# Optimization experiments

Measured on AMD Instinct MI355X. Metric: run time of the kernel, lower is better.

## Reference

```python
import jax, jax.numpy as jnp
import numpy as np

D_MODEL = 1024
NUM_HEADS = 16
DEPTH = D_MODEL // NUM_HEADS


def setup_inputs() -> dict:
    key = jax.random.key(0)
    ks = jax.random.split(key, 11)
    B, S = 4, 2048
    scale = 1.0 / np.sqrt(D_MODEL)
    inp = {
        "q": jax.random.normal(ks[0], (B, S, D_MODEL), jnp.float32),
        "k": jax.random.normal(ks[1], (B, S, D_MODEL), jnp.float32),
        "v": jax.random.normal(ks[2], (B, S, D_MODEL), jnp.float32),
        # Linear params (weight stored [out, in] like torch; applied as x @ W.T + b)
        "wq_w": jax.random.normal(ks[3], (D_MODEL, D_MODEL), jnp.float32) * scale,
        "wq_b": jnp.zeros((D_MODEL,), jnp.float32),
        "wk_w": jax.random.normal(ks[4], (D_MODEL, D_MODEL), jnp.float32) * scale,
        "wk_b": jnp.zeros((D_MODEL,), jnp.float32),
        "wv_w": jax.random.normal(ks[5], (D_MODEL, D_MODEL), jnp.float32) * scale,
        "wv_b": jnp.zeros((D_MODEL,), jnp.float32),
        "wo_w": jax.random.normal(ks[6], (D_MODEL, D_MODEL), jnp.float32) * scale,
        "wo_b": jnp.zeros((D_MODEL,), jnp.float32),
    }
    return inp


def _split_heads(x, B, S):
    # [B, S, D] -> [B, H, S, depth]
    return x.reshape(B, S, NUM_HEADS, DEPTH).transpose(0, 2, 1, 3)


def reference(q, k, v, wq_w, wq_b, wk_w, wk_b, wv_w, wv_b, wo_w, wo_b):
    B, S, _ = q.shape
    qh = _split_heads(q @ wq_w.T + wq_b, B, S)
    kh = _split_heads(k @ wk_w.T + wk_b, B, S)
    vh = _split_heads(v @ wv_w.T + wv_b, B, S)
    # scaled dot-product attention: [B, H, Sq, Sk]
    scores = jnp.einsum("bhqd,bhkd->bhqk", qh, kh) / jnp.sqrt(
        jnp.asarray(DEPTH, qh.dtype))
    attn = jax.nn.softmax(scores, axis=-1)
    ctx = jnp.einsum("bhqk,bhkd->bhqd", attn, vh)
    # [B, H, S, depth] -> [B, S, D]
    ctx = ctx.transpose(0, 2, 1, 3).reshape(B, S, D_MODEL)
    return ctx @ wo_w.T + wo_b
```

## Files before the change

kernel.cpp:

```cpp
#include <hip/hip_runtime.h>
#include <hip/hip_bf16.h>

typedef __attribute__((ext_vector_type(8))) short bf16x8;
typedef __attribute__((ext_vector_type(4))) short bf16x4;
typedef __attribute__((ext_vector_type(4))) float f32x4;
typedef __attribute__((address_space(3))) ushort lds_ushort;

#define MFMA32(a, b, c) __builtin_amdgcn_mfma_f32_16x16x32_bf16(a, b, c, 0, 0, 0)
#if __has_builtin(__builtin_amdgcn_mfma_f32_16x16x16bf16_1k)
#define HAVE_MFMA16K 1
#define MFMA16K(a, b, c) __builtin_amdgcn_mfma_f32_16x16x16bf16_1k(a, b, c, 0, 0, 0)
#else
#define HAVE_MFMA16K 0
#endif

#define ASYNC16(g, l)                                                          \
    __builtin_amdgcn_global_load_lds(                                          \
        (const __attribute__((address_space(1))) unsigned int*)(g),            \
        (__attribute__((address_space(3))) unsigned int*)(l), 16, 0, 0)

#define TR16(dst, addr, OFF)                                                   \
    asm volatile("ds_read_b64_tr_b16 %0, %1 offset:%2"                         \
                 : "=v"(dst) : "v"(addr), "i"(OFF))

__device__ __forceinline__ ushort f2bf(float f) {
    __hip_bfloat16 h = __float2bfloat16(f);
    return *reinterpret_cast<ushort*>(&h);
}
__device__ __forceinline__ uint cvtpk(float a, float b) {
    uint r;
    asm("v_cvt_pk_bf16_f32 %0, %1, %2" : "=v"(r) : "v"(a), "v"(b));
    return r;
}

#define QSCALE 0.18033688011112042f

struct CvtArgs { const float* s[7]; ushort* d[7]; int nb[7]; };

__global__ __launch_bounds__(256) void cvtk(CvtArgs a) {
    const int z = blockIdx.y;
    if ((int)blockIdx.x >= a.nb[z]) return;
    const float* s = a.s[z];
    ushort* d = a.d[z];
    const size_t i = (size_t)blockIdx.x * 2048 + threadIdx.x * 8;
    float4 f0 = *(const float4*)&s[i];
    float4 f1 = *(const float4*)&s[i + 4];
    *(ushort4*)&d[i]     = make_ushort4(f2bf(f0.x), f2bf(f0.y), f2bf(f0.z), f2bf(f0.w));
    *(ushort4*)&d[i + 4] = make_ushort4(f2bf(f1.x), f2bf(f1.y), f2bf(f1.z), f2bf(f1.w));
}

struct GemmArgs {
    const ushort* X[3]; const ushort* W[3]; const float* B[3];
    void* O[3]; int mode[3]; float scale[3];
};

__global__ __launch_bounds__(256) void gemm3(GemmArgs g) {
    __shared__ __attribute__((aligned(16))) ushort As[2][128][32];
    __shared__ __attribute__((aligned(16))) ushort Bs[2][128][32];

    const int z = blockIdx.z;
    const ushort* __restrict__ X = g.X[z];
    const ushort* __restrict__ W = g.W[z];
    const float*  __restrict__ bias = g.B[z];
    const int mode = g.mode[z];
    const float scale = g.scale[z];

    const int tid  = threadIdx.x;
    const int lane = tid & 63;
    const int wave = tid >> 6;
    const int quad = lane >> 4;
    const int l16  = lane & 15;
    const int wm   = (wave >> 1) * 64;
    const int wn   = (wave & 1) * 64;

    const int flat = blockIdx.x + 8 * blockIdx.y;
    const int t    = (flat & 7) * 64 + (flat >> 3);
    const int m0   = (t >> 3) * 128;
    const int n0   = (t & 7) * 128;

    f32x4 acc[4][4];
#pragma unroll
    for (int i = 0; i < 4; i++)
#pragma unroll
        for (int j = 0; j < 4; j++) acc[i][j] = (f32x4)0.0f;

    auto stage = [&](int buf, int k0) {
#pragma unroll
        for (int j = 0; j < 2; j++) {
            const int c   = j * 256 + tid;
            const int r   = c >> 2;
            const int col = (c & 3) * 8;
            ASYNC16(&X[(size_t)(m0 + r) * 1024 + k0 + col],
                    &As[buf][0][0] + (size_t)(j * 256 + wave * 64) * 8);
            ASYNC16(&W[(size_t)(n0 + r) * 1024 + k0 + col],
                    &Bs[buf][0][0] + (size_t)(j * 256 + wave * 64) * 8);
        }
    };

    stage(0, 0);
    stage(1, 32);
    int cur = 0;

    for (int k0 = 0; k0 < 1024; k0 += 32) {
        if (k0 < 1024 - 32) {
            asm volatile("s_waitcnt vmcnt(4)" ::: "memory");
        } else {
            asm volatile("s_waitcnt vmcnt(0)" ::: "memory");
        }
        __builtin_amdgcn_s_barrier();
        __builtin_amdgcn_sched_barrier(0);

        bf16x8 af[4], bfr[4];
#pragma unroll
        for (int i = 0; i < 4; i++)
            af[i] = *(const bf16x8*)&As[cur][wm + i * 16 + l16][quad * 8];
#pragma unroll
        for (int j = 0; j < 4; j++)
            bfr[j] = *(const bf16x8*)&Bs[cur][wn + j * 16 + l16][quad * 8];
        asm volatile("s_waitcnt lgkmcnt(0)" ::: "memory");
        __builtin_amdgcn_sched_barrier(0);
        __builtin_amdgcn_s_barrier();
        __builtin_amdgcn_sched_barrier(0);
        if (k0 + 64 < 1024) stage(cur, k0 + 64);

#pragma unroll
        for (int i = 0; i < 4; i++)
#pragma unroll
            for (int j = 0; j < 4; j++)
                acc[i][j] = MFMA32(af[i], bfr[j], acc[i][j]);
        cur ^= 1;
    }

#pragma unroll
    for (int i = 0; i < 4; i++) {
#pragma unroll
        for (int j = 0; j < 4; j++) {
            const int n  = n0 + wn + j * 16 + l16;
            const float bb = bias[n];
#pragma unroll
            for (int r = 0; r < 4; r++) {
                const int m = m0 + wm + i * 16 + quad * 4 + r;
                const float val = (acc[i][j][r] + bb) * scale;
                if (mode == 2) {
                    ((float*)g.O[z])[(size_t)m * 1024 + n] = val;
                } else {
                    const int bat = m >> 11, s = m & 2047, h = n >> 6, d = n & 63;
                    ((ushort*)g.O[z])[((size_t)((bat * 16 + h) * 2048 + s)) * 64 + d]
                        = f2bf(val);
                }
            }
        }
    }
}

__global__ __launch_bounds__(256, 4) void attn(
    const ushort* __restrict__ Qp, const ushort* __restrict__ Kp,
    const ushort* __restrict__ Vp, ushort* __restrict__ ctx)
{
    __shared__ __attribute__((aligned(16))) ushort Ks[2][2 * 64 * 32];
    __shared__ __attribute__((aligned(16))) ushort Vs[2][64 * 64];

    const int tid  = threadIdx.x;
    const int lane = tid & 63;
    const int wave = tid >> 6;
    const int quad = lane >> 4;
    const int l16  = lane & 15;

    const int id = blockIdx.x;
    const int bh = (id & 7) * 8 + ((id >> 3) & 7);
    const int q0 = (id >> 6) * 128;
    const int b  = bh >> 4, h = bh & 15;

    const ushort* Qg = Qp + ((size_t)bh * 2048 + q0) * 64;
    const ushort* Kg = Kp + (size_t)bh * 2048 * 64;
    const ushort* Vg = Vp + (size_t)bh * 2048 * 64;

    bf16x8 aq[2][2];
#pragma unroll
    for (int st = 0; st < 2; st++)
#pragma unroll
        for (int kk = 0; kk < 2; kk++)
            aq[st][kk] = *(const bf16x8*)&Qg[(size_t)(wave * 32 + st * 16 + l16) * 64
                                            + kk * 32 + quad * 8];

    f32x4 o[2][4];
#pragma unroll
    for (int st = 0; st < 2; st++)
#pragma unroll
        for (int jd = 0; jd < 4; jd++) o[st][jd] = (f32x4)0.0f;
#if HAVE_MFMA16K
    f32x4 ls[2] = {(f32x4)0.0f, (f32x4)0.0f};
    union { uint u[2]; bf16x4 v; } ones;
    ones.u[0] = 0x3F803F80u; ones.u[1] = 0x3F803F80u;
#else
    float lsum[2] = {0.f, 0.f};
#endif

    auto stage = [&](int buf, int n0) {
#pragma unroll
        for (int j = 0; j < 2; j++) {
            const int c    = j * 256 + tid;
            const int colq = c & 3;
            const int row  = (c >> 2) & 63;
            const int half = c >> 8;
            ASYNC16(&Kg[(size_t)(n0 + row) * 64 + half * 32 + colq * 8],
                    &Ks[buf][0] + (size_t)(j * 256 + wave * 64) * 8);
        }
#pragma unroll
        for (int j = 0; j < 2; j++) {
            const int c   = j * 256 + tid;
            const int key = ((c >> 5) << 2) | ((c >> 1) & 3);
            const int d   = (((c >> 3) & 3) << 4) | ((c & 1) << 3);
            ASYNC16(&Vg[(size_t)(n0 + key) * 64 + d],
                    &Vs[buf][0] + (size_t)(j * 256 + wave * 64) * 8);
        }
    };

    stage(0, 0);
    int cur = 0;

    for (int n0 = 0; n0 < 2048; n0 += 64) {
        __syncthreads();
        if (n0 + 64 < 2048) stage(cur ^ 1, n0 + 64);

        uint pk[4][2][2];
#pragma unroll
        for (int kb = 0; kb < 4; kb++) {
            bf16x8 kf0 = *(const bf16x8*)&Ks[cur][(size_t)(kb * 16 + l16) * 32 + quad * 8];
            bf16x8 kf1 = *(const bf16x8*)&Ks[cur][(size_t)(64 + kb * 16 + l16) * 32 + quad * 8];
#pragma unroll
            for (int st = 0; st < 2; st++) {
                f32x4 s = (f32x4)0.0f;
                s = MFMA32(kf0, aq[st][0], s);
                s = MFMA32(kf1, aq[st][1], s);
                float e0 = __builtin_amdgcn_exp2f(s[0]);
                float e1 = __builtin_amdgcn_exp2f(s[1]);
                float e2 = __builtin_amdgcn_exp2f(s[2]);
                float e3 = __builtin_amdgcn_exp2f(s[3]);
                pk[kb][st][0] = cvtpk(e0, e1);
                pk[kb][st][1] = cvtpk(e2, e3);
#if !HAVE_MFMA16K
                lsum[st] += (e0 + e1) + (e2 + e3);
#endif
            }
        }

#if HAVE_MFMA16K
        const lds_ushort* vp = (const lds_ushort*)&Vs[cur][0] + quad * 256 + l16 * 4;
        bf16x4 vf[4][4];
#define TRISSUE(JD)                                                            \
        TR16(vf[JD][0], vp, (JD) * 128 + 0);                                   \
        TR16(vf[JD][1], vp, (JD) * 128 + 2048);                                \
        TR16(vf[JD][2], vp, (JD) * 128 + 4096);                                \
        TR16(vf[JD][3], vp, (JD) * 128 + 6144);
        TRISSUE(0) TRISSUE(1) TRISSUE(2) TRISSUE(3)

#pragma unroll
        for (int kb = 0; kb < 4; kb++) {
#pragma unroll
            for (int st = 0; st < 2; st++) {
                union { uint u[2]; bf16x4 v; } pf;
                pf.u[0] = pk[kb][st][0];
                pf.u[1] = pk[kb][st][1];
                ls[st] = MFMA16K(pf.v, ones.v, ls[st]);
            }
        }

#define PVWAIT(N)                                                              \
        asm volatile("s_waitcnt lgkmcnt(" #N ")" ::: "memory");                \
        __builtin_amdgcn_sched_barrier(0);
#define PVJD(JD)                                                               \
        _Pragma("unroll")                                                      \
        for (int kb = 0; kb < 4; kb++) {                                       \
            _Pragma("unroll")                                                  \
            for (int st = 0; st < 2; st++) {                                   \
                union { uint u[2]; bf16x4 v; } pf;                             \
                pf.u[0] = pk[kb][st][0];                                       \
                pf.u[1] = pk[kb][st][1];                                       \
                o[st][JD] = MFMA16K(pf.v, vf[JD][kb], o[st][JD]);              \
            }                                                                  \
        }
        __builtin_amdgcn_s_setprio(1);
        PVWAIT(12) PVJD(0)
        PVWAIT(8)  PVJD(1)
        PVWAIT(4)  PVJD(2)
        PVWAIT(0)  PVJD(3)
        __builtin_amdgcn_s_setprio(0);
#else
        const int addr0 = 4 * ((2 * (quad & 1)) * 16 + l16);
        const int addr1 = addr0 + 64;
#pragma unroll
        for (int kt = 0; kt < 2; kt++) {
            bf16x8 apf[2];
#pragma unroll
            for (int st = 0; st < 2; st++) {
                union { uint u[4]; bf16x8 v; } t;
#pragma unroll
                for (int j = 0; j < 4; j++) {
                    uint src = (quad & 2) ? pk[kt * 2 + 1][st][j & 1]
                                          : pk[kt * 2][st][j & 1];
                    t.u[j] = (uint)__builtin_amdgcn_ds_bpermute(
                        (j >> 1) ? addr1 : addr0, (int)src);
                }
                apf[st] = t.v;
            }
#pragma unroll
            for (int jd = 0; jd < 4; jd++) {
                union { ushort s[8]; bf16x8 v; } vv;
#pragma unroll
                for (int e = 0; e < 8; e++) {
                    const int key = kt * 32 + quad * 8 + e;
                    const int d   = jd * 16 + l16;
                    vv.s[e] = Vs[cur][(key >> 2) * 256 + (d >> 4) * 64
                                      + (key & 3) * 16 + (d & 15)];
                }
#pragma unroll
                for (int st = 0; st < 2; st++)
                    o[st][jd] = MFMA32(apf[st], vv.v, o[st][jd]);
            }
        }
#endif
        cur ^= 1;
    }

#if HAVE_MFMA16K
#pragma unroll
    for (int st = 0; st < 2; st++) {
        float inv[4];
#pragma unroll
        for (int r = 0; r < 4; r++) inv[r] = 1.0f / ls[st][r];
#pragma unroll
        for (int jd = 0; jd < 4; jd++) {
#pragma unroll
            for (int r = 0; r < 4; r++) {
                const int s = q0 + wave * 32 + st * 16 + quad * 4 + r;
                ctx[((size_t)(b * 2048 + s)) * 1024 + h * 64 + jd * 16 + l16] =
                    f2bf(o[st][jd][r] * inv[r]);
            }
        }
    }
#else
#pragma unroll
    for (int st = 0; st < 2; st++) {
        float lsv = lsum[st];
        lsv += __shfl_xor(lsv, 16, 64);
        lsv += __shfl_xor(lsv, 32, 64);
        float inv[4];
#pragma unroll
        for (int r = 0; r < 4; r++)
            inv[r] = 1.0f / __shfl(lsv, quad * 4 + r, 64);
#pragma unroll
        for (int jd = 0; jd < 4; jd++) {
#pragma unroll
            for (int r = 0; r < 4; r++) {
                const int s = q0 + wave * 32 + st * 16 + quad * 4 + r;
                ctx[((size_t)(b * 2048 + s)) * 1024 + h * 64 + jd * 16 + l16] =
                    f2bf(o[st][jd][r] * inv[r]);
            }
        }
    }
#endif
}

extern "C" void kernel_launch(void* const* d_in, const int* in_sizes, int n_in,
                              void* d_out, int out_size, void* d_ws, size_t ws_size,
                              hipStream_t stream) {
    const float* q    = (const float*)d_in[0];
    const float* k    = (const float*)d_in[1];
    const float* v    = (const float*)d_in[2];
    const float* wq_w = (const float*)d_in[3];
    const float* wq_b = (const float*)d_in[4];
    const float* wk_w = (const float*)d_in[5];
    const float* wk_b = (const float*)d_in[6];
    const float* wv_w = (const float*)d_in[7];
    const float* wv_b = (const float*)d_in[8];
    const float* wo_w = (const float*)d_in[9];
    const float* wo_b = (const float*)d_in[10];
    float* out = (float*)d_out;

    const size_t NE = (size_t)4 * 2048 * 1024;
    const size_t NW = (size_t)1024 * 1024;
    const size_t need_fused = (6 * NE + 4 * NW) * 2;

    dim3 blk(256);

    if (ws_size >= need_fused) {
        ushort* Xq = (ushort*)d_ws;
        ushort* Xk = Xq + NE;
        ushort* Xv = Xk + NE;
        ushort* Wq = Xv + NE;
        ushort* Wk = Wq + NW;
        ushort* Wv = Wk + NW;
        ushort* Wo = Wv + NW;
        ushort* Qp = Wo + NW;
        ushort* Kp = Qp + NE;
        ushort* Vp = Kp + NE;
        ushort* ctx = Xq;

        CvtArgs ca;
        ca.s[0]=q;    ca.d[0]=Xq; ca.nb[0]=4096;
        ca.s[1]=k;    ca.d[1]=Xk; ca.nb[1]=4096;
        ca.s[2]=v;    ca.d[2]=Xv; ca.nb[2]=4096;
        ca.s[3]=wq_w; ca.d[3]=Wq; ca.nb[3]=512;
        ca.s[4]=wk_w; ca.d[4]=Wk; ca.nb[4]=512;
        ca.s[5]=wv_w; ca.d[5]=Wv; ca.nb[5]=512;
        ca.s[6]=wo_w; ca.d[6]=Wo; ca.nb[6]=512;
        cvtk<<<dim3(4096, 7), blk, 0, stream>>>(ca);

        GemmArgs ga;
        ga.X[0]=Xq; ga.W[0]=Wq; ga.B[0]=wq_b; ga.O[0]=Qp; ga.mode[0]=0; ga.scale[0]=QSCALE;
        ga.X[1]=Xk; ga.W[1]=Wk; ga.B[1]=wk_b; ga.O[1]=Kp; ga.mode[1]=0; ga.scale[1]=1.0f;
        ga.X[2]=Xv; ga.W[2]=Wv; ga.B[2]=wv_b; ga.O[2]=Vp; ga.mode[2]=0; ga.scale[2]=1.0f;
        gemm3<<<dim3(8, 64, 3), blk, 0, stream>>>(ga);

        attn<<<dim3(1024), blk, 0, stream>>>(Qp, Kp, Vp, ctx);

        GemmArgs go;
        go.X[0]=ctx; go.W[0]=Wo; go.B[0]=wo_b; go.O[0]=out; go.mode[0]=2; go.scale[0]=1.0f;
        go.X[1]=go.X[0]; go.W[1]=go.W[0]; go.B[1]=go.B[0]; go.O[1]=go.O[0]; go.mode[1]=2; go.scale[1]=1.0f;
        go.X[2]=go.X[0]; go.W[2]=go.W[0]; go.B[2]=go.B[0]; go.O[2]=go.O[0]; go.mode[2]=2; go.scale[2]=1.0f;
        gemm3<<<dim3(8, 64, 1), blk, 0, stream>>>(go);
    } else {
        ushort* Xb  = (ushort*)d_ws;
        ushort* Wb  = Xb + NE;
        ushort* Wob = Wb + NW;
        ushort* Qp  = Wob + NW;
        ushort* Kp  = Qp + NE;
        ushort* Vp  = Kp + NE;
        ushort* ctx = Xb;

        CvtArgs c0;
        c0.s[0]=q;    c0.d[0]=Xb;  c0.nb[0]=4096;
        c0.s[1]=wq_w; c0.d[1]=Wb;  c0.nb[1]=512;
        c0.s[2]=wo_w; c0.d[2]=Wob; c0.nb[2]=512;
        for (int i = 3; i < 7; i++) { c0.s[i]=q; c0.d[i]=Xb; c0.nb[i]=0; }
        cvtk<<<dim3(4096, 3), blk, 0, stream>>>(c0);
        GemmArgs ga;
        for (int i = 0; i < 3; i++) { ga.X[i]=Xb; ga.W[i]=Wb; ga.B[i]=wq_b; ga.O[i]=Qp; ga.mode[i]=0; ga.scale[i]=QSCALE; }
        gemm3<<<dim3(8, 64, 1), blk, 0, stream>>>(ga);

        CvtArgs c1;
        c1.s[0]=k;    c1.d[0]=Xb; c1.nb[0]=4096;
        c1.s[1]=wk_w; c1.d[1]=Wb; c1.nb[1]=512;
        for (int i = 2; i < 7; i++) { c1.s[i]=k; c1.d[i]=Xb; c1.nb[i]=0; }
        cvtk<<<dim3(4096, 2), blk, 0, stream>>>(c1);
        GemmArgs gb;
        for (int i = 0; i < 3; i++) { gb.X[i]=Xb; gb.W[i]=Wb; gb.B[i]=wk_b; gb.O[i]=Kp; gb.mode[i]=0; gb.scale[i]=1.0f; }
        gemm3<<<dim3(8, 64, 1), blk, 0, stream>>>(gb);

        CvtArgs c2;
        c2.s[0]=v;    c2.d[0]=Xb; c2.nb[0]=4096;
        c2.s[1]=wv_w; c2.d[1]=Wb; c2.nb[1]=512;
        for (int i = 2; i < 7; i++) { c2.s[i]=v; c2.d[i]=Xb; c2.nb[i]=0; }
        cvtk<<<dim3(4096, 2), blk, 0, stream>>>(c2);
        GemmArgs gc;
        for (int i = 0; i < 3; i++) { gc.X[i]=Xb; gc.W[i]=Wb; gc.B[i]=wv_b; gc.O[i]=Vp; gc.mode[i]=0; gc.scale[i]=1.0f; }
        gemm3<<<dim3(8, 64, 1), blk, 0, stream>>>(gc);

        attn<<<dim3(1024), blk, 0, stream>>>(Qp, Kp, Vp, ctx);

        GemmArgs go;
        for (int i = 0; i < 3; i++) { go.X[i]=ctx; go.W[i]=Wob; go.B[i]=wo_b; go.O[i]=out; go.mode[i]=2; go.scale[i]=1.0f; }
        gemm3<<<dim3(8, 64, 1), blk, 0, stream>>>(go);
    }
}
```

Baseline: 338.4 us.

## Fuse fp32-to-bf16 activation conversion into QKV projection GEMM loads

The separate conversion pass over the q/k/v activations is removed. The QKV GEMM now loads fp32 rows directly, converts them to bf16 in registers with packed cvt, and writes them into LDS, prefetching one tile ahead. Only the weights are still pre-converted. This removes a full write and reread of three activation tensors, but the A operand now goes through registers instead of async global-to-LDS loads. The bf16 GEMM path also drops its hand-tuned vmcnt waits in favour of a simpler __syncthreads double buffer, which may add stalls.

```diff
diff --git a/kernel.cpp b/kernel.cpp
--- a/kernel.cpp
+++ b/kernel.cpp
@@ -35,7 +35,7 @@
 
 #define QSCALE 0.18033688011112042f
 
-struct CvtArgs { const float* s[7]; ushort* d[7]; int nb[7]; };
+struct CvtArgs { const float* s[4]; ushort* d[4]; int nb[4]; };
 
 __global__ __launch_bounds__(256) void cvtk(CvtArgs a) {
     const int z = blockIdx.y;
@@ -50,8 +50,8 @@
 }
 
 struct GemmArgs {
-    const ushort* X[3]; const ushort* W[3]; const float* B[3];
-    void* O[3]; int mode[3]; float scale[3];
+    const ushort* X[3]; const float* Xf[3]; const ushort* W[3];
+    const float* B[3]; void* O[3]; int mode[3]; int xf32[3]; float scale[3];
 };
 
 __global__ __launch_bounds__(256) void gemm3(GemmArgs g) {
@@ -59,7 +59,6 @@
     __shared__ __attribute__((aligned(16))) ushort Bs[2][128][32];
 
     const int z = blockIdx.z;
-    const ushort* __restrict__ X = g.X[z];
     const ushort* __restrict__ W = g.W[z];
     const float*  __restrict__ bias = g.B[z];
     const int mode = g.mode[z];
@@ -84,51 +83,100 @@
 #pragma unroll
         for (int j = 0; j < 4; j++) acc[i][j] = (f32x4)0.0f;
 
-    auto stage = [&](int buf, int k0) {
+    auto stageB = [&](int buf, int k0) {
 #pragma unroll
         for (int j = 0; j < 2; j++) {
             const int c   = j * 256 + tid;
             const int r   = c >> 2;
             const int col = (c & 3) * 8;
-            ASYNC16(&X[(size_t)(m0 + r) * 1024 + k0 + col],
-                    &As[buf][0][0] + (size_t)(j * 256 + wave * 64) * 8);
             ASYNC16(&W[(size_t)(n0 + r) * 1024 + k0 + col],
                     &Bs[buf][0][0] + (size_t)(j * 256 + wave * 64) * 8);
         }
     };
 
-    stage(0, 0);
-    stage(1, 32);
-    int cur = 0;
-
-    for (int k0 = 0; k0 < 1024; k0 += 32) {
-        if (k0 < 1024 - 32) {
-            asm volatile("s_waitcnt vmcnt(4)" ::: "memory");
-        } else {
-            asm volatile("s_waitcnt vmcnt(0)" ::: "memory");
-        }
-        __builtin_amdgcn_s_barrier();
-        __builtin_amdgcn_sched_barrier(0);
-
-        bf16x8 af[4], bfr[4];
-#pragma unroll
-        for (int i = 0; i < 4; i++)
-            af[i] = *(const bf16x8*)&As[cur][wm + i * 16 + l16][quad * 8];
-#pragma unroll
-        for (int j = 0; j < 4; j++)
-            bfr[j] = *(const bf16x8*)&Bs[cur][wn + j * 16 + l16][quad * 8];
-        asm volatile("s_waitcnt lgkmcnt(0)" ::: "memory");
-        __builtin_amdgcn_sched_barrier(0);
-        __builtin_amdgcn_s_barrier();
-        __builtin_amdgcn_sched_barrier(0);
-        if (k0 + 64 < 1024) stage(cur, k0 + 64);
-
-#pragma unroll
-        for (int i = 0; i < 4; i++)
+    if (g.xf32[z]) {
+        const float* __restrict__ Xf = g.Xf[z];
+        const int r0 = tid >> 2, cq = (tid & 3) * 8;
+        float4 a0, a1, b0, b1;
+        auto loadA = [&](int k0) {
+            a0 = *(const float4*)&Xf[(size_t)(m0 + r0) * 1024 + k0 + cq];
+            a1 = *(const float4*)&Xf[(size_t)(m0 + r0) * 1024 + k0 + cq + 4];
+            b0 = *(const float4*)&Xf[(size_t)(m0 + 64 + r0) * 1024 + k0 + cq];
+            b1 = *(const float4*)&Xf[(size_t)(m0 + 64 + r0) * 1024 + k0 + cq + 4];
+        };
+        auto writeA = [&](int buf) {
+            uint4 w;
+            w.x = cvtpk(a0.x, a0.y); w.y = cvtpk(a0.z, a0.w);
+            w.z = cvtpk(a1.x, a1.y); w.w = cvtpk(a1.z, a1.w);
+            *(uint4*)&As[buf][r0][cq] = w;
+            w.x = cvtpk(b0.x, b0.y); w.y = cvtpk(b0.z, b0.w);
+            w.z = cvtpk(b1.x, b1.y); w.w = cvtpk(b1.z, b1.w);
+            *(uint4*)&As[buf][64 + r0][cq] = w;
+        };
+
+        loadA(0);
+        writeA(0);
+        stageB(0, 0);
+        loadA(32);
+
+        int cur = 0;
+        for (int k0 = 0; k0 < 1024; k0 += 32) {
+            __syncthreads();
+            if (k0 + 32 < 1024) {
+                writeA(cur ^ 1);
+                stageB(cur ^ 1, k0 + 32);
+            }
+            if (k0 + 64 < 1024) loadA(k0 + 64);
+
+            bf16x8 af[4], bfr[4];
+#pragma unroll
+            for (int i = 0; i < 4; i++)
+                af[i] = *(const bf16x8*)&As[cur][wm + i * 16 + l16][quad * 8];
 #pragma unroll
             for (int j = 0; j < 4; j++)
-                acc[i][j] = MFMA32(af[i], bfr[j], acc[i][j]);
-        cur ^= 1;
+                bfr[j] = *(const bf16x8*)&Bs[cur][wn + j * 16 + l16][quad * 8];
+#pragma unroll
+            for (int i = 0; i < 4; i++)
+#pragma unroll
+                for (int j = 0; j < 4; j++)
+                    acc[i][j] = MFMA32(af[i], bfr[j], acc[i][j]);
+            cur ^= 1;
+        }
+    } else {
+        const ushort* __restrict__ X = g.X[z];
+        auto stageA = [&](int buf, int k0) {
+#pragma unroll
+            for (int j = 0; j < 2; j++) {
+                const int c   = j * 256 + tid;
+                const int r   = c >> 2;
+                const int col = (c & 3) * 8;
+                ASYNC16(&X[(size_t)(m0 + r) * 1024 + k0 + col],
+                        &As[buf][0][0] + (size_t)(j * 256 + wave * 64) * 8);
+            }
+        };
+        stageA(0, 0);
+        stageB(0, 0);
+        int cur = 0;
+        for (int k0 = 0; k0 < 1024; k0 += 32) {
+            __syncthreads();
+            if (k0 + 32 < 1024) {
+                stageA(cur ^ 1, k0 + 32);
+                stageB(cur ^ 1, k0 + 32);
+            }
+            bf16x8 af[4], bfr[4];
+#pragma unroll
+            for (int i = 0; i < 4; i++)
+                af[i] = *(const bf16x8*)&As[cur][wm + i * 16 + l16][quad * 8];
+#pragma unroll
+            for (int j = 0; j < 4; j++)
+                bfr[j] = *(const bf16x8*)&Bs[cur][wn + j * 16 + l16][quad * 8];
+#pragma unroll
+            for (int i = 0; i < 4; i++)
+#pragma unroll
+                for (int j = 0; j < 4; j++)
+                    acc[i][j] = MFMA32(af[i], bfr[j], acc[i][j]);
+            cur ^= 1;
+        }
     }
 
 #pragma unroll
@@ -380,87 +428,82 @@
 
     const size_t NE = (size_t)4 * 2048 * 1024;
     const size_t NW = (size_t)1024 * 1024;
-    const size_t need_fused = (6 * NE + 4 * NW) * 2;
+    const size_t need_fused = (4 * NE + 4 * NW) * 2;
 
     dim3 blk(256);
 
     if (ws_size >= need_fused) {
-        ushort* Xq = (ushort*)d_ws;
-        ushort* Xk = Xq + NE;
-        ushort* Xv = Xk + NE;
-        ushort* Wq = Xv + NE;
+        ushort* Wq = (ushort*)d_ws;
         ushort* Wk = Wq + NW;
         ushort* Wv = Wk + NW;
         ushort* Wo = Wv + NW;
         ushort* Qp = Wo + NW;
         ushort* Kp = Qp + NE;
         ushort* Vp = Kp + NE;
-        ushort* ctx = Xq;
+        ushort* ctx = Vp + NE;
 
         CvtArgs ca;
-        ca.s[0]=q;    ca.d[0]=Xq; ca.nb[0]=4096;
-        ca.s[1]=k;    ca.d[1]=Xk; ca.nb[1]=4096;
-        ca.s[2]=v;    ca.d[2]=Xv; ca.nb[2]=4096;
-        ca.s[3]=wq_w; ca.d[3]=Wq; ca.nb[3]=512;
-        ca.s[4]=wk_w; ca.d[4]=Wk; ca.nb[4]=512;
-        ca.s[5]=wv_w; ca.d[5]=Wv; ca.nb[5]=512;
-        ca.s[6]=wo_w; ca.d[6]=Wo; ca.nb[6]=512;
-        cvtk<<<dim3(4096, 7), blk, 0, stream>>>(ca);
+        ca.s[0]=wq_w; ca.d[0]=Wq; ca.nb[0]=512;
+        ca.s[1]=wk_w; ca.d[1]=Wk; ca.nb[1]=512;
+        ca.s[2]=wv_w; ca.d[2]=Wv; ca.nb[2]=512;
+        ca.s[3]=wo_w; ca.d[3]=Wo; ca.nb[3]=512;
+        cvtk<<<dim3(512, 4), blk, 0, stream>>>(ca);
 
         GemmArgs ga;
-        ga.X[0]=Xq; ga.W[0]=Wq; ga.B[0]=wq_b; ga.O[0]=Qp; ga.mode[0]=0; ga.scale[0]=QSCALE;
-        ga.X[1]=Xk; ga.W[1]=Wk; ga.B[1]=wk_b; ga.O[1]=Kp; ga.mode[1]=0; ga.scale[1]=1.0f;
-        ga.X[2]=Xv; ga.W[2]=Wv; ga.B[2]=wv_b; ga.O[2]=Vp; ga.mode[2]=0; ga.scale[2]=1.0f;
+        ga.Xf[0]=q; ga.Xf[1]=k; ga.Xf[2]=v;
+        ga.X[0]=ga.X[1]=ga.X[2]=nullptr;
+        ga.W[0]=Wq; ga.W[1]=Wk; ga.W[2]=Wv;
+        ga.B[0]=wq_b; ga.B[1]=wk_b; ga.B[2]=wv_b;
+        ga.O[0]=Qp; ga.O[1]=Kp; ga.O[2]=Vp;
+        ga.mode[0]=ga.mode[1]=ga.mode[2]=0;
+        ga.xf32[0]=ga.xf32[1]=ga.xf32[2]=1;
+        ga.scale[0]=QSCALE; ga.scale[1]=1.0f; ga.scale[2]=1.0f;
         gemm3<<<dim3(8, 64, 3), blk, 0, stream>>>(ga);
 
         attn<<<dim3(1024), blk, 0, stream>>>(Qp, Kp, Vp, ctx);
 
         GemmArgs go;
-        go.X[0]=ctx; go.W[0]=Wo; go.B[0]=wo_b; go.O[0]=out; go.mode[0]=2; go.scale[0]=1.0f;
-        go.X[1]=go.X[0]; go.W[1]=go.W[0]; go.B[1]=go.B[0]; go.O[1]=go.O[0]; go.mode[1]=2; go.scale[1]=1.0f;
-        go.X[2]=go.X[0]; go.W[2]=go.W[0]; go.B[2]=go.B[0]; go.O[2]=go.O[0]; go.mode[2]=2; go.scale[2]=1.0f;
+        for (int i = 0; i < 3; i++) {
+            go.X[i]=ctx; go.Xf[i]=nullptr; go.W[i]=Wo; go.B[i]=wo_b;
+            go.O[i]=out; go.mode[i]=2; go.xf32[i]=0; go.scale[i]=1.0f;
+        }
         gemm3<<<dim3(8, 64, 1), blk, 0, stream>>>(go);
     } else {
-        ushort* Xb  = (ushort*)d_ws;
-        ushort* Wb  = Xb + NE;
-        ushort* Wob = Wb + NW;
-        ushort* Qp  = Wob + NW;
+        ushort* Qp  = (ushort*)d_ws;
         ushort* Kp  = Qp + NE;
         ushort* Vp  = Kp + NE;
-        ushort* ctx = Xb;
-
-        CvtArgs c0;
-        c0.s[0]=q;    c0.d[0]=Xb;  c0.nb[0]=4096;
-        c0.s[1]=wq_w; c0.d[1]=Wb;  c0.nb[1]=512;
-        c0.s[2]=wo_w; c0.d[2]=Wob; c0.nb[2]=512;
-        for (int i = 3; i < 7; i++) { c0.s[i]=q; c0.d[i]=Xb; c0.nb[i]=0; }
-        cvtk<<<dim3(4096, 3), blk, 0, stream>>>(c0);
-        GemmArgs ga;
-        for (int i = 0; i < 3; i++) { ga.X[i]=Xb; ga.W[i]=Wb; ga.B[i]=wq_b; ga.O[i]=Qp; ga.mode[i]=0; ga.scale[i]=QSCALE; }
-        gemm3<<<dim3(8, 64, 1), blk, 0, stream>>>(ga);
-
-        CvtArgs c1;
-        c1.s[0]=k;    c1.d[0]=Xb; c1.nb[0]=4096;
-        c1.s[1]=wk_w; c1.d[1]=Wb; c1.nb[1]=512;
-        for (int i = 2; i < 7; i++) { c1.s[i]=k; c1.d[i]=Xb; c1.nb[i]=0; }
-        cvtk<<<dim3(4096, 2), blk, 0, stream>>>(c1);
-        GemmArgs gb;
-        for (int i = 0; i < 3; i++) { gb.X[i]=Xb; gb.W[i]=Wb; gb.B[i]=wk_b; gb.O[i]=Kp; gb.mode[i]=0; gb.scale[i]=1.0f; }
-        gemm3<<<dim3(8, 64, 1), blk, 0, stream>>>(gb);
-
-        CvtArgs c2;
-        c2.s[0]=v;    c2.d[0]=Xb; c2.nb[0]=4096;
-        c2.s[1]=wv_w; c2.d[1]=Wb; c2.nb[1]=512;
-        for (int i = 2; i < 7; i++) { c2.s[i]=v; c2.d[i]=Xb; c2.nb[i]=0; }
-        cvtk<<<dim3(4096, 2), blk, 0, stream>>>(c2);
-        GemmArgs gc;
-        for (int i = 0; i < 3; i++) { gc.X[i]=Xb; gc.W[i]=Wb; gc.B[i]=wv_b; gc.O[i]=Vp; gc.mode[i]=0; gc.scale[i]=1.0f; }
-        gemm3<<<dim3(8, 64, 1), blk, 0, stream>>>(gc);
+        ushort* ctx = Vp + NE;
+        ushort* Wb  = ctx + NE;
+
+        const float* xs[3] = {q, k, v};
+        const float* ws[3] = {wq_w, wk_w, wv_w};
+        const float* bs[3] = {wq_b, wk_b, wv_b};
+        ushort* os[3] = {Qp, Kp, Vp};
+        for (int p = 0; p < 3; p++) {
+            CvtArgs c;
+            c.s[0]=ws[p]; c.d[0]=Wb; c.nb[0]=512;
+            for (int i = 1; i < 4; i++) { c.s[i]=ws[p]; c.d[i]=Wb; c.nb[i]=0; }
+            cvtk<<<dim3(512, 1), blk, 0, stream>>>(c);
+            GemmArgs gg;
+            for (int i = 0; i < 3; i++) {
+                gg.Xf[i]=xs[p]; gg.X[i]=nullptr; gg.W[i]=Wb; gg.B[i]=bs[p];
+                gg.O[i]=os[p]; gg.mode[i]=0; gg.xf32[i]=1;
+                gg.scale[i]=(p == 0) ? QSCALE : 1.0f;
+            }
+            gemm3<<<dim3(8, 64, 1), blk, 0, stream>>>(gg);
+        }
 
         attn<<<dim3(1024), blk, 0, stream>>>(Qp, Kp, Vp, ctx);
 
+        CvtArgs c;
+        c.s[0]=wo_w; c.d[0]=Wb; c.nb[0]=512;
+        for (int i = 1; i < 4; i++) { c.s[i]=wo_w; c.d[i]=Wb; c.nb[i]=0; }
+        cvtk<<<dim3(512, 1), blk, 0, stream>>>(c);
         GemmArgs go;
-        for (int i = 0; i < 3; i++) { go.X[i]=ctx; go.W[i]=Wob; go.B[i]=wo_b; go.O[i]=out; go.mode[i]=2; go.scale[i]=1.0f; }
+        for (int i = 0; i < 3; i++) {
+            go.X[i]=ctx; go.Xf[i]=nullptr; go.W[i]=Wb; go.B[i]=wo_b;
+            go.O[i]=out; go.mode[i]=2; go.xf32[i]=0; go.scale[i]=1.0f;
+        }
         gemm3<<<dim3(8, 64, 1), blk, 0, stream>>>(go);
     }
 }
```

Result: slower. 366.6 us (+8.3%).

## Replace 128x128 GEMM with 256x256-tile 8-wave kernel with swizzled LDS and deeper pipeline

Applied to the files above, without the earlier changes.

Replaces the 128x128x32 projection GEMM (4 waves, 2-stage buffer) with a 256x256x64 tile kernel of 8 waves using 128 KB of dynamic LDS. Loads are split into quarter-tile chunks issued across sub-steps, and LDS columns are XOR-swizzled to avoid bank conflicts. MFMA blocks are wrapped in s_setprio. The larger tile is meant to raise arithmetic intensity and cut global traffic per FLOP, but the grid shrinks to 128 blocks per projection, which leaves part of the machine idle and limits occupancy. The fallback path is also reorganized to convert Wo after attention.

```diff
diff --git a/kernel.cpp b/kernel.cpp
--- a/kernel.cpp
+++ b/kernel.cpp
@@ -54,9 +54,8 @@
     void* O[3]; int mode[3]; float scale[3];
 };
 
-__global__ __launch_bounds__(256) void gemm3(GemmArgs g) {
-    __shared__ __attribute__((aligned(16))) ushort As[2][128][32];
-    __shared__ __attribute__((aligned(16))) ushort Bs[2][128][32];
+__global__ __launch_bounds__(512, 2) void gemm256(GemmArgs g) {
+    extern __shared__ __attribute__((aligned(16))) ushort smem[];
 
     const int z = blockIdx.z;
     const ushort* __restrict__ X = g.X[z];
@@ -68,79 +67,106 @@
     const int tid  = threadIdx.x;
     const int lane = tid & 63;
     const int wave = tid >> 6;
-    const int quad = lane >> 4;
+    const int quad = (lane >> 4) & 3;
     const int l16  = lane & 15;
-    const int wm   = (wave >> 1) * 64;
-    const int wn   = (wave & 1) * 64;
-
-    const int flat = blockIdx.x + 8 * blockIdx.y;
-    const int t    = (flat & 7) * 64 + (flat >> 3);
-    const int m0   = (t >> 3) * 128;
-    const int n0   = (t & 7) * 128;
-
-    f32x4 acc[4][4];
-#pragma unroll
-    for (int i = 0; i < 4; i++)
+    const int wm   = (wave >> 2) * 128;
+    const int wn   = (wave & 3) * 64;
+
+    const int flat = blockIdx.x + 4 * blockIdx.y;
+    const int t0   = (flat & 7) * 16 + (flat >> 3);
+    const int m0   = (t0 >> 2) * 256;
+    const int n0   = (t0 & 3) * 256;
+
+    f32x4 acc[8][4];
+#pragma unroll
+    for (int i = 0; i < 8; i++)
 #pragma unroll
         for (int j = 0; j < 4; j++) acc[i][j] = (f32x4)0.0f;
 
-    auto stage = [&](int buf, int k0) {
+    auto issue = [&](int s) {
+        if (s >= 64) return;
+        const int tile = s >> 2;
+        const int buf  = tile & 1;
+        const int kind = s & 3;
+        const int k0   = tile * 64;
+        const int half = kind & 1;
+        const bool isB = (kind < 2);
+        const ushort* src = isB ? W : X;
+        const int base    = isB ? n0 : m0;
+        ushort* dst = smem + (isB ? 32768 : 0) + buf * 16384;
 #pragma unroll
         for (int j = 0; j < 2; j++) {
-            const int c   = j * 256 + tid;
-            const int r   = c >> 2;
-            const int col = (c & 3) * 8;
-            ASYNC16(&X[(size_t)(m0 + r) * 1024 + k0 + col],
-                    &As[buf][0][0] + (size_t)(j * 256 + wave * 64) * 8);
-            ASYNC16(&W[(size_t)(n0 + r) * 1024 + k0 + col],
-                    &Bs[buf][0][0] + (size_t)(j * 256 + wave * 64) * 8);
+            const int c   = half * 1024 + j * 512 + tid;
+            const int row = c >> 3;
+            const int gp  = (c & 7) ^ (row & 7);
+            ASYNC16(&src[(size_t)(base + row) * 1024 + k0 + gp * 8],
+                    dst + (size_t)(half * 1024 + j * 512 + wave * 64) * 8);
         }
     };
 
-    stage(0, 0);
-    stage(1, 32);
-    int cur = 0;
-
-    for (int k0 = 0; k0 < 1024; k0 += 32) {
-        if (k0 < 1024 - 32) {
-            asm volatile("s_waitcnt vmcnt(4)" ::: "memory");
-        } else {
-            asm volatile("s_waitcnt vmcnt(0)" ::: "memory");
-        }
-        __builtin_amdgcn_s_barrier();
-        __builtin_amdgcn_sched_barrier(0);
-
-        bf16x8 af[4], bfr[4];
-#pragma unroll
-        for (int i = 0; i < 4; i++)
-            af[i] = *(const bf16x8*)&As[cur][wm + i * 16 + l16][quad * 8];
-#pragma unroll
-        for (int j = 0; j < 4; j++)
-            bfr[j] = *(const bf16x8*)&Bs[cur][wn + j * 16 + l16][quad * 8];
-        asm volatile("s_waitcnt lgkmcnt(0)" ::: "memory");
-        __builtin_amdgcn_sched_barrier(0);
-        __builtin_amdgcn_s_barrier();
-        __builtin_amdgcn_sched_barrier(0);
-        if (k0 + 64 < 1024) stage(cur, k0 + 64);
-
-#pragma unroll
-        for (int i = 0; i < 4; i++)
-#pragma unroll
-            for (int j = 0; j < 4; j++)
-                acc[i][j] = MFMA32(af[i], bfr[j], acc[i][j]);
-        cur ^= 1;
-    }
-
-#pragma unroll
-    for (int i = 0; i < 4; i++) {
-#pragma unroll
-        for (int j = 0; j < 4; j++) {
-            const int n  = n0 + wn + j * 16 + l16;
+    for (int s = 0; s < 6; s++) issue(s);
+    asm volatile("s_waitcnt vmcnt(4)" ::: "memory");
+    __builtin_amdgcn_sched_barrier(0);
+    __builtin_amdgcn_s_barrier();
+
+    const int sw = l16 & 7;
+
+    for (int t = 0; t < 16; t++) {
+        const ushort* A  = smem + (t & 1) * 16384;
+        const ushort* Bm = smem + 32768 + (t & 1) * 16384;
+        bf16x8 bfrag[4][2];
+#pragma unroll
+        for (int p = 0; p < 4; p++) {
+            issue(4 * t + p + 6);
+            if (p == 0) {
+#pragma unroll
+                for (int nj = 0; nj < 4; nj++)
+#pragma unroll
+                    for (int ks = 0; ks < 2; ks++)
+                        bfrag[nj][ks] = *(const bf16x8*)
+                            &Bm[(size_t)(wn + nj * 16 + l16) * 64
+                                + (((ks * 4 + quad) ^ sw) * 8)];
+            }
+            bf16x8 af[2][2];
+#pragma unroll
+            for (int i = 0; i < 2; i++)
+#pragma unroll
+                for (int ks = 0; ks < 2; ks++)
+                    af[i][ks] = *(const bf16x8*)
+                        &A[(size_t)(wm + (2 * p + i) * 16 + l16) * 64
+                           + (((ks * 4 + quad) ^ sw) * 8)];
+            __builtin_amdgcn_s_barrier();
+            asm volatile("s_waitcnt lgkmcnt(0)" ::: "memory");
+            __builtin_amdgcn_sched_barrier(0);
+            __builtin_amdgcn_s_setprio(1);
+#pragma unroll
+            for (int i = 0; i < 2; i++)
+#pragma unroll
+                for (int nj = 0; nj < 4; nj++) {
+                    acc[2 * p + i][nj] = MFMA32(af[i][0], bfrag[nj][0],
+                                                acc[2 * p + i][nj]);
+                    acc[2 * p + i][nj] = MFMA32(af[i][1], bfrag[nj][1],
+                                                acc[2 * p + i][nj]);
+                }
+            __builtin_amdgcn_s_setprio(0);
+            if (p == 3) {
+                asm volatile("s_waitcnt vmcnt(4)" ::: "memory");
+                __builtin_amdgcn_sched_barrier(0);
+            }
+            __builtin_amdgcn_s_barrier();
+        }
+    }
+
+#pragma unroll
+    for (int mi = 0; mi < 8; mi++) {
+#pragma unroll
+        for (int nj = 0; nj < 4; nj++) {
+            const int n  = n0 + wn + nj * 16 + l16;
             const float bb = bias[n];
 #pragma unroll
             for (int r = 0; r < 4; r++) {
-                const int m = m0 + wm + i * 16 + quad * 4 + r;
-                const float val = (acc[i][j][r] + bb) * scale;
+                const int m = m0 + wm + mi * 16 + quad * 4 + r;
+                const float val = (acc[mi][nj][r] + bb) * scale;
                 if (mode == 2) {
                     ((float*)g.O[z])[(size_t)m * 1024 + n] = val;
                 } else {
@@ -381,8 +407,12 @@
     const size_t NE = (size_t)4 * 2048 * 1024;
     const size_t NW = (size_t)1024 * 1024;
     const size_t need_fused = (6 * NE + 4 * NW) * 2;
+    const size_t LDSB = 131072;
 
     dim3 blk(256);
+    dim3 gblk(512);
+    dim3 ggrid(4, 32, 3);
+    dim3 ggrid1(4, 32, 1);
 
     if (ws_size >= need_fused) {
         ushort* Xq = (ushort*)d_ws;
@@ -411,15 +441,16 @@
         ga.X[0]=Xq; ga.W[0]=Wq; ga.B[0]=wq_b; ga.O[0]=Qp; ga.mode[0]=0; ga.scale[0]=QSCALE;
         ga.X[1]=Xk; ga.W[1]=Wk; ga.B[1]=wk_b; ga.O[1]=Kp; ga.mode[1]=0; ga.scale[1]=1.0f;
         ga.X[2]=Xv; ga.W[2]=Wv; ga.B[2]=wv_b; ga.O[2]=Vp; ga.mode[2]=0; ga.scale[2]=1.0f;
-        gemm3<<<dim3(8, 64, 3), blk, 0, stream>>>(ga);
+        gemm256<<<ggrid, gblk, LDSB, stream>>>(ga);
 
         attn<<<dim3(1024), blk, 0, stream>>>(Qp, Kp, Vp, ctx);
 
         GemmArgs go;
-        go.X[0]=ctx; go.W[0]=Wo; go.B[0]=wo_b; go.O[0]=out; go.mode[0]=2; go.scale[0]=1.0f;
-        go.X[1]=go.X[0]; go.W[1]=go.W[0]; go.B[1]=go.B[0]; go.O[1]=go.O[0]; go.mode[1]=2; go.scale[1]=1.0f;
-        go.X[2]=go.X[0]; go.W[2]=go.W[0]; go.B[2]=go.B[0]; go.O[2]=go.O[0]; go.mode[2]=2; go.scale[2]=1.0f;
-        gemm3<<<dim3(8, 64, 1), blk, 0, stream>>>(go);
+        for (int i = 0; i < 3; i++) {
+            go.X[i]=ctx; go.W[i]=Wo; go.B[i]=wo_b;
+            go.O[i]=out; go.mode[i]=2; go.scale[i]=1.0f;
+        }
+        gemm256<<<ggrid1, gblk, LDSB, stream>>>(go);
     } else {
         ushort* Xb  = (ushort*)d_ws;
         ushort* Wb  = Xb + NE;
@@ -429,38 +460,35 @@
         ushort* Vp  = Kp + NE;
         ushort* ctx = Xb;
 
-        CvtArgs c0;
-        c0.s[0]=q;    c0.d[0]=Xb;  c0.nb[0]=4096;
-        c0.s[1]=wq_w; c0.d[1]=Wb;  c0.nb[1]=512;
-        c0.s[2]=wo_w; c0.d[2]=Wob; c0.nb[2]=512;
-        for (int i = 3; i < 7; i++) { c0.s[i]=q; c0.d[i]=Xb; c0.nb[i]=0; }
-        cvtk<<<dim3(4096, 3), blk, 0, stream>>>(c0);
-        GemmArgs ga;
-        for (int i = 0; i < 3; i++) { ga.X[i]=Xb; ga.W[i]=Wb; ga.B[i]=wq_b; ga.O[i]=Qp; ga.mode[i]=0; ga.scale[i]=QSCALE; }
-        gemm3<<<dim3(8, 64, 1), blk, 0, stream>>>(ga);
-
-        CvtArgs c1;
-        c1.s[0]=k;    c1.d[0]=Xb; c1.nb[0]=4096;
-        c1.s[1]=wk_w; c1.d[1]=Wb; c1.nb[1]=512;
-        for (int i = 2; i < 7; i++) { c1.s[i]=k; c1.d[i]=Xb; c1.nb[i]=0; }
-        cvtk<<<dim3(4096, 2), blk, 0, stream>>>(c1);
-        GemmArgs gb;
-        for (int i = 0; i < 3; i++) { gb.X[i]=Xb; gb.W[i]=Wb; gb.B[i]=wk_b; gb.O[i]=Kp; gb.mode[i]=0; gb.scale[i]=1.0f; }
-        gemm3<<<dim3(8, 64, 1), blk, 0, stream>>>(gb);
-
-        CvtArgs c2;
-        c2.s[0]=v;    c2.d[0]=Xb; c2.nb[0]=4096;
-        c2.s[1]=wv_w; c2.d[1]=Wb; c2.nb[1]=512;
-        for (int i = 2; i < 7; i++) { c2.s[i]=v; c2.d[i]=Xb; c2.nb[i]=0; }
-        cvtk<<<dim3(4096, 2), blk, 0, stream>>>(c2);
-        GemmArgs gc;
-        for (int i = 0; i < 3; i++) { gc.X[i]=Xb; gc.W[i]=Wb; gc.B[i]=wv_b; gc.O[i]=Vp; gc.mode[i]=0; gc.scale[i]=1.0f; }
-        gemm3<<<dim3(8, 64, 1), blk, 0, stream>>>(gc);
+        const float* xs[3] = {q, k, v};
+        const float* ws[3] = {wq_w, wk_w, wv_w};
+        const float* bs[3] = {wq_b, wk_b, wv_b};
+        ushort* os[3] = {Qp, Kp, Vp};
+        for (int p = 0; p < 3; p++) {
+            CvtArgs c;
+            c.s[0]=xs[p]; c.d[0]=Xb; c.nb[0]=4096;
+            c.s[1]=ws[p]; c.d[1]=Wb; c.nb[1]=512;
+            for (int i = 2; i < 7; i++) { c.s[i]=xs[p]; c.d[i]=Xb; c.nb[i]=0; }
+            cvtk<<<dim3(4096, 2), blk, 0, stream>>>(c);
+            GemmArgs gg;
+            for (int i = 0; i < 3; i++) {
+                gg.X[i]=Xb; gg.W[i]=Wb; gg.B[i]=bs[p]; gg.O[i]=os[p];
+                gg.mode[i]=0; gg.scale[i]=(p == 0) ? QSCALE : 1.0f;
+            }
+            gemm256<<<ggrid1, gblk, LDSB, stream>>>(gg);
+        }
 
         attn<<<dim3(1024), blk, 0, stream>>>(Qp, Kp, Vp, ctx);
 
+        CvtArgs c;
+        c.s[0]=wo_w; c.d[0]=Wob; c.nb[0]=512;
+        for (int i = 1; i < 7; i++) { c.s[i]=wo_w; c.d[i]=Wob; c.nb[i]=0; }
+        cvtk<<<dim3(512, 1), blk, 0, stream>>>(c);
         GemmArgs go;
-        for (int i = 0; i < 3; i++) { go.X[i]=ctx; go.W[i]=Wob; go.B[i]=wo_b; go.O[i]=out; go.mode[i]=2; go.scale[i]=1.0f; }
-        gemm3<<<dim3(8, 64, 1), blk, 0, stream>>>(go);
-    }
-}
+        for (int i = 0; i < 3; i++) {
+            go.X[i]=ctx; go.W[i]=Wob; go.B[i]=wo_b;
+            go.O[i]=out; go.mode[i]=2; go.scale[i]=1.0f;
+        }
+        gemm256<<<ggrid1, gblk, LDSB, stream>>>(go);
+    }
+}
```

Result: no change. 345.1 us (+2.0%).
